# Kernel optimization log

Hardware: AMD Instinct MI355X
Metric: run time of the kernel (lower is better)

Reference implementation:

```python
import jax, jax.numpy as jnp
import numpy as np

N_KNOTS = 8
LATENT = 16
DEGREE = 3


def _de_boor(x, t, c, p):
    # x: arbitrary-shape query points; t: (n_knots+6,) padded knots; c: (n_knots+2,) control points
    k = jnp.digitize(x, t) - 1  # interval index per element (binary search gather)
    d = [c[k + (j - p)] for j in range(p + 1)]
    for r in range(1, p + 1):
        for j in range(p, r - 1, -1):
            t_lo = t[k + (j - p)]
            t_hi = t[k + (j + 1 - r)]
            alpha = (x - t_lo) / (t_hi - t_lo)
            d[j] = (1.0 - alpha) * d[j - 1] + alpha * d[j]
    return d[p]


def setup_inputs() -> dict:
    key = jax.random.key(0)
    ks = jax.random.split(key, 8)
    # |k| grid normalized to fftfreq range: values in [0, sqrt(3)]
    x = jax.random.uniform(ks[0], (256, 256, 256), dtype=jnp.float32) * 1.7320508
    a = jax.random.uniform(ks[1], (1,), dtype=jnp.float32)  # scale factor in (0,1)
    inv = 1.0 / np.sqrt(LATENT).astype(np.float32)
    W1 = jax.random.normal(ks[2], (1, LATENT), jnp.float32)
    b1 = jnp.zeros((LATENT,), jnp.float32)
    W2 = jax.random.normal(ks[3], (LATENT, LATENT), jnp.float32) * inv
    b2 = jnp.zeros((LATENT,), jnp.float32)
    Ww = jax.random.normal(ks[4], (LATENT, N_KNOTS + 1), jnp.float32) * inv
    bw = jnp.zeros((N_KNOTS + 1,), jnp.float32)
    Wk = jax.random.normal(ks[5], (LATENT, N_KNOTS - 1), jnp.float32) * inv
    bk = jnp.zeros((N_KNOTS - 1,), jnp.float32)
    return {"x": x, "a": a, "W1": W1, "b1": b1, "W2": W2, "b2": b2,
            "Ww": Ww, "bw": bw, "Wk": Wk, "bk": bk}


def reference(x, a, W1, b1, W2, b2, Ww, bw, Wk, bk):
    # tiny MLP on scalar a -> spline weights w and knot increments k
    net = jnp.sin(a @ W1 + b1)           # (LATENT,)
    net = jnp.sin(net @ W2 + b2)         # (LATENT,)
    w = net @ Ww + bw                    # (N_KNOTS+1,)
    kk = net @ Wk + bk                   # (N_KNOTS-1,)
    kk = jnp.concatenate([jnp.zeros((1,), x.dtype), jnp.cumsum(jax.nn.softmax(kk))])  # (N_KNOTS,), monotone in [0,1]
    w = jnp.concatenate([jnp.zeros((1,), x.dtype), w])                                 # (N_KNOTS+2,)
    ak = jnp.concatenate([jnp.zeros((3,), x.dtype), kk, jnp.ones((3,), x.dtype)])      # padded knots
    xq = jnp.clip(x / jnp.sqrt(jnp.asarray(3.0, x.dtype)), 0.0, 1.0 - 0.0001)
    return _de_boor(xq, ak, w, DEGREE)
```

## Files before the change

kernel.cpp:

```cpp
#include <hip/hip_runtime.h>
#include <math.h>

typedef float f4 __attribute__((ext_vector_type(4)));

__global__ void nsf_params_kernel(const float* __restrict__ a,
                                  const float* __restrict__ W1, const float* __restrict__ b1,
                                  const float* __restrict__ W2, const float* __restrict__ b2,
                                  const float* __restrict__ Ww, const float* __restrict__ bw,
                                  const float* __restrict__ Wk, const float* __restrict__ bk,
                                  float* __restrict__ ws)
{
    __shared__ float n1[16], n2[16], wv[9], krs[7], t[14], cc[10], d3[7], p0[4];
    const int tid = threadIdx.x;

    if (tid < 16) n1[tid] = sinf(a[0] * W1[tid] + b1[tid]);
    __syncthreads();

    if (tid < 16) {
        float s = b2[tid];
        for (int i = 0; i < 16; ++i) s += n1[i] * W2[i * 16 + tid];
        n2[tid] = sinf(s);
    }
    __syncthreads();

    if (tid < 9) {
        float s = bw[tid];
        for (int i = 0; i < 16; ++i) s += n2[i] * Ww[i * 9 + tid];
        wv[tid] = s;
    }
    if (tid >= 16 && tid < 23) {
        const int j = tid - 16;
        float s = bk[j];
        for (int i = 0; i < 16; ++i) s += n2[i] * Wk[i * 7 + j];
        krs[j] = s;
    }
    __syncthreads();

    if (tid == 0) {
        float m = krs[0];
        for (int j = 1; j < 7; ++j) m = fmaxf(m, krs[j]);
        float e[7], se = 0.f;
        for (int j = 0; j < 7; ++j) { e[j] = expf(krs[j] - m); se += e[j]; }
        const float inv = 1.f / se;
        t[0] = t[1] = t[2] = t[3] = 0.f;
        float cum = 0.f;
        for (int j = 0; j < 7; ++j) { cum += e[j] * inv; t[4 + j] = cum; }
        t[11] = t[12] = t[13] = 1.f;
        cc[0] = 0.f;
        for (int j = 0; j < 9; ++j) cc[1 + j] = wv[j];
    }
    __syncthreads();

    if (tid < 7) {
        const int k = 3 + tid;
        const float tk = t[k];
        float d[4][4];
        for (int j = 0; j < 4; ++j) {
            d[j][0] = cc[k - 3 + j];
            d[j][1] = d[j][2] = d[j][3] = 0.f;
        }
        for (int r = 1; r <= 3; ++r) {
            for (int j = 3; j >= r; --j) {
                const float tlo = t[k + j - 3];
                const float thi = t[k + j + 1 - r];
                const float B = 1.f / (thi - tlo);
                const float A = (tk - tlo) * B;
                float nd[4];
                for (int nn = 0; nn < 4; ++nn) nd[nn] = d[j - 1][nn];
                for (int nn = 0; nn < r; ++nn) {
                    const float en = d[j][nn] - d[j - 1][nn];
                    nd[nn]     += A * en;
                    nd[nn + 1] += B * en;
                }
                for (int nn = 0; nn < 4; ++nn) d[j][nn] = nd[nn];
            }
        }
        d3[tid] = d[3][3];
        if (tid == 0) {
            p0[0] = d[3][0]; p0[1] = d[3][1]; p0[2] = d[3][2]; p0[3] = d[3][3];
        }
    }
    __syncthreads();

    if (tid < 16) {
        float val;
        if (tid < 4)       val = p0[tid];
        else if (tid < 10) val = t[tid];
        else               val = d3[tid - 9] - d3[tid - 10];
        ws[tid] = val;
    }
}

__device__ __forceinline__ float eval_one(float xv,
                                          float c0, float c1, float c2, float c3,
                                          float k1, float k2, float k3,
                                          float k4, float k5, float k6,
                                          float e1, float e2, float e3,
                                          float e4, float e5, float e6)
{
    const float xq = fminf(fmaxf(xv * 0.57735026918962576f, 0.0f), 0.9999f);
    float acc = fmaf(fmaf(fmaf(c3, xq, c2), xq, c1), xq, c0);
    float r;
    r = fmaxf(xq - k1, 0.f); acc = fmaf(e1 * r, r * r, acc);
    r = fmaxf(xq - k2, 0.f); acc = fmaf(e2 * r, r * r, acc);
    r = fmaxf(xq - k3, 0.f); acc = fmaf(e3 * r, r * r, acc);
    r = fmaxf(xq - k4, 0.f); acc = fmaf(e4 * r, r * r, acc);
    r = fmaxf(xq - k5, 0.f); acc = fmaf(e5 * r, r * r, acc);
    r = fmaxf(xq - k6, 0.f); acc = fmaf(e6 * r, r * r, acc);
    return acc;
}

__global__ __launch_bounds__(256) void nsf_eval_kernel(const float* __restrict__ x,
                                                       const float* __restrict__ ws,
                                                       float* __restrict__ out, int n)
{
    const float c0 = ws[0],  c1 = ws[1],  c2 = ws[2],  c3 = ws[3];
    const float k1 = ws[4],  k2 = ws[5],  k3 = ws[6],  k4 = ws[7],  k5 = ws[8],  k6 = ws[9];
    const float e1 = ws[10], e2 = ws[11], e3 = ws[12], e4 = ws[13], e5 = ws[14], e6 = ws[15];

    const int n4 = n >> 2;
    const int gid = blockIdx.x * blockDim.x + threadIdx.x;
    const int stride = gridDim.x * blockDim.x;

    const f4* __restrict__ x4 = reinterpret_cast<const f4*>(x);
    f4* __restrict__ o4 = reinterpret_cast<f4*>(out);

    for (int idx = gid; idx < n4; idx += stride) {
        const f4 v = x4[idx];
        f4 r;
        r.x = eval_one(v.x, c0,c1,c2,c3, k1,k2,k3,k4,k5,k6, e1,e2,e3,e4,e5,e6);
        r.y = eval_one(v.y, c0,c1,c2,c3, k1,k2,k3,k4,k5,k6, e1,e2,e3,e4,e5,e6);
        r.z = eval_one(v.z, c0,c1,c2,c3, k1,k2,k3,k4,k5,k6, e1,e2,e3,e4,e5,e6);
        r.w = eval_one(v.w, c0,c1,c2,c3, k1,k2,k3,k4,k5,k6, e1,e2,e3,e4,e5,e6);
        __builtin_nontemporal_store(r, o4 + idx);
    }
    for (int j = (n4 << 2) + gid; j < n; j += stride)
        out[j] = eval_one(x[j], c0,c1,c2,c3, k1,k2,k3,k4,k5,k6, e1,e2,e3,e4,e5,e6);
}

extern "C" void kernel_launch(void* const* d_in, const int* in_sizes, int n_in,
                              void* d_out, int out_size, void* d_ws, size_t ws_size,
                              hipStream_t stream)
{
    const float* x  = (const float*)d_in[0];
    const float* a  = (const float*)d_in[1];
    const float* W1 = (const float*)d_in[2];
    const float* b1 = (const float*)d_in[3];
    const float* W2 = (const float*)d_in[4];
    const float* b2 = (const float*)d_in[5];
    const float* Ww = (const float*)d_in[6];
    const float* bw = (const float*)d_in[7];
    const float* Wk = (const float*)d_in[8];
    const float* bk = (const float*)d_in[9];
    float* out = (float*)d_out;
    float* ws  = (float*)d_ws;
    const int n = out_size;

    hipLaunchKernelGGL(nsf_params_kernel, dim3(1), dim3(64), 0, stream,
                       a, W1, b1, W2, b2, Ww, bw, Wk, bk, ws);

    hipLaunchKernelGGL(nsf_eval_kernel, dim3(2048), dim3(256), 0, stream,
                       x, ws, out, n);
}
```

Baseline: 129.8 us.

## Fuse parameter MLP into eval kernel, recomputing spline coefficients per block

Drops the separate single-block parameter kernel. Each of the 2048 blocks now recomputes the tiny MLP, softmax knots and piecewise-cubic coefficients into shared memory, then evaluates its share of the grid. This removes one kernel launch and the serial dependency between the two launches. The cost is redundant per-block setup work and several __syncthreads before streaming begins. The input load is also switched to a nontemporal load.

```diff
diff --git a/kernel.cpp b/kernel.cpp
--- a/kernel.cpp
+++ b/kernel.cpp
@@ -3,14 +3,36 @@
 
 typedef float f4 __attribute__((ext_vector_type(4)));
 
-__global__ void nsf_params_kernel(const float* __restrict__ a,
-                                  const float* __restrict__ W1, const float* __restrict__ b1,
-                                  const float* __restrict__ W2, const float* __restrict__ b2,
-                                  const float* __restrict__ Ww, const float* __restrict__ bw,
-                                  const float* __restrict__ Wk, const float* __restrict__ bk,
-                                  float* __restrict__ ws)
+
+__device__ __forceinline__ float eval_one(float xv,
+                                          float c0, float c1, float c2, float c3,
+                                          float k1, float k2, float k3,
+                                          float k4, float k5, float k6,
+                                          float e1, float e2, float e3,
+                                          float e4, float e5, float e6)
 {
-    __shared__ float n1[16], n2[16], wv[9], krs[7], t[14], cc[10], d3[7], p0[4];
+    const float xq = fminf(fmaxf(xv * 0.57735026918962576f, 0.0f), 0.9999f);
+    float acc = fmaf(fmaf(fmaf(c3, xq, c2), xq, c1), xq, c0);
+    float r;
+    r = fmaxf(xq - k1, 0.f); acc = fmaf(e1 * r, r * r, acc);
+    r = fmaxf(xq - k2, 0.f); acc = fmaf(e2 * r, r * r, acc);
+    r = fmaxf(xq - k3, 0.f); acc = fmaf(e3 * r, r * r, acc);
+    r = fmaxf(xq - k4, 0.f); acc = fmaf(e4 * r, r * r, acc);
+    r = fmaxf(xq - k5, 0.f); acc = fmaf(e5 * r, r * r, acc);
+    r = fmaxf(xq - k6, 0.f); acc = fmaf(e6 * r, r * r, acc);
+    return acc;
+}
+
+__global__ __launch_bounds__(256) void nsf_fused_kernel(
+        const float* __restrict__ x,
+        const float* __restrict__ a,
+        const float* __restrict__ W1, const float* __restrict__ b1,
+        const float* __restrict__ W2, const float* __restrict__ b2,
+        const float* __restrict__ Ww, const float* __restrict__ bw,
+        const float* __restrict__ Wk, const float* __restrict__ bk,
+        float* __restrict__ out, int n)
+{
+    __shared__ float n1[16], n2[16], wv[9], krs[7], t[14], cc[10], d3[7], p0[4], P[16];
     const int tid = threadIdx.x;
 
     if (tid < 16) n1[tid] = sinf(a[0] * W1[tid] + b1[tid]);
@@ -87,46 +109,23 @@
         if (tid < 4)       val = p0[tid];
         else if (tid < 10) val = t[tid];
         else               val = d3[tid - 9] - d3[tid - 10];
-        ws[tid] = val;
+        P[tid] = val;
     }
-}
+    __syncthreads();
 
-__device__ __forceinline__ float eval_one(float xv,
-                                          float c0, float c1, float c2, float c3,
-                                          float k1, float k2, float k3,
-                                          float k4, float k5, float k6,
-                                          float e1, float e2, float e3,
-                                          float e4, float e5, float e6)
-{
-    const float xq = fminf(fmaxf(xv * 0.57735026918962576f, 0.0f), 0.9999f);
-    float acc = fmaf(fmaf(fmaf(c3, xq, c2), xq, c1), xq, c0);
-    float r;
-    r = fmaxf(xq - k1, 0.f); acc = fmaf(e1 * r, r * r, acc);
-    r = fmaxf(xq - k2, 0.f); acc = fmaf(e2 * r, r * r, acc);
-    r = fmaxf(xq - k3, 0.f); acc = fmaf(e3 * r, r * r, acc);
-    r = fmaxf(xq - k4, 0.f); acc = fmaf(e4 * r, r * r, acc);
-    r = fmaxf(xq - k5, 0.f); acc = fmaf(e5 * r, r * r, acc);
-    r = fmaxf(xq - k6, 0.f); acc = fmaf(e6 * r, r * r, acc);
-    return acc;
-}
-
-__global__ __launch_bounds__(256) void nsf_eval_kernel(const float* __restrict__ x,
-                                                       const float* __restrict__ ws,
-                                                       float* __restrict__ out, int n)
-{
-    const float c0 = ws[0],  c1 = ws[1],  c2 = ws[2],  c3 = ws[3];
-    const float k1 = ws[4],  k2 = ws[5],  k3 = ws[6],  k4 = ws[7],  k5 = ws[8],  k6 = ws[9];
-    const float e1 = ws[10], e2 = ws[11], e3 = ws[12], e4 = ws[13], e5 = ws[14], e6 = ws[15];
+    const float c0 = P[0],  c1 = P[1],  c2 = P[2],  c3 = P[3];
+    const float k1 = P[4],  k2 = P[5],  k3 = P[6],  k4 = P[7],  k5 = P[8],  k6 = P[9];
+    const float e1 = P[10], e2 = P[11], e3 = P[12], e4 = P[13], e5 = P[14], e6 = P[15];
 
     const int n4 = n >> 2;
-    const int gid = blockIdx.x * blockDim.x + threadIdx.x;
+    const int gid = blockIdx.x * blockDim.x + tid;
     const int stride = gridDim.x * blockDim.x;
 
     const f4* __restrict__ x4 = reinterpret_cast<const f4*>(x);
     f4* __restrict__ o4 = reinterpret_cast<f4*>(out);
 
     for (int idx = gid; idx < n4; idx += stride) {
-        const f4 v = x4[idx];
+        const f4 v = __builtin_nontemporal_load(x4 + idx);
         f4 r;
         r.x = eval_one(v.x, c0,c1,c2,c3, k1,k2,k3,k4,k5,k6, e1,e2,e3,e4,e5,e6);
         r.y = eval_one(v.y, c0,c1,c2,c3, k1,k2,k3,k4,k5,k6, e1,e2,e3,e4,e5,e6);
@@ -153,12 +152,8 @@
     const float* Wk = (const float*)d_in[8];
     const float* bk = (const float*)d_in[9];
     float* out = (float*)d_out;
-    float* ws  = (float*)d_ws;
     const int n = out_size;
 
-    hipLaunchKernelGGL(nsf_params_kernel, dim3(1), dim3(64), 0, stream,
-                       a, W1, b1, W2, b2, Ww, bw, Wk, bk, ws);
-
-    hipLaunchKernelGGL(nsf_eval_kernel, dim3(2048), dim3(256), 0, stream,
-                       x, ws, out, n);
+    hipLaunchKernelGGL(nsf_fused_kernel, dim3(2048), dim3(256), 0, stream,
+                       x, a, W1, b1, W2, b2, Ww, bw, Wk, bk, out, n);
 }
```

New measurement: 138.6 us. +6.8%, slower.
